# Optimization experiments

Measured on AMD Instinct MI355X. Metric: run time of the kernel, lower is better.

The kernel has to match this reference:

```python
import jax, jax.numpy as jnp
import numpy as np

BN_EPS = 1e-5

def _batchnorm(x, gamma, beta):
    # torch BatchNorm1d in training mode: batch mean, biased variance
    mean = jnp.mean(x, axis=0)
    var = jnp.mean(jnp.square(x - mean), axis=0)
    return (x - mean) * jax.lax.rsqrt(var + BN_EPS) * gamma + beta

def setup_inputs() -> dict:
    key = jax.random.key(0)
    ks = jax.random.split(key, 6)
    N, E, D_atom, D_nbr = 50000, 1600000, 64, 64
    d_in, d_out = 2 * D_atom + D_nbr, 2 * D_atom  # 192, 128
    return {
        "atom_in_fea": jax.random.normal(ks[0], (N, D_atom), dtype=jnp.float32),
        "nbr_fea": jax.random.normal(ks[1], (E, D_nbr), dtype=jnp.float32),
        "edge_src": jax.random.randint(ks[2], (E,), 0, N),
        "edge_dst": jax.random.randint(ks[3], (E,), 0, N),
        "W": jax.random.normal(ks[4], (d_in, d_out), dtype=jnp.float32) * (1.0 / np.sqrt(d_in)),
        "b": jax.random.normal(ks[5], (d_out,), dtype=jnp.float32) * 0.01,
        "bn1_gamma": jnp.ones((d_out,), dtype=jnp.float32),
        "bn1_beta": jnp.zeros((d_out,), dtype=jnp.float32),
        "bn2_gamma": jnp.ones((D_atom,), dtype=jnp.float32),
        "bn2_beta": jnp.zeros((D_atom,), dtype=jnp.float32),
    }

def reference(atom_in_fea, nbr_fea, edge_src, edge_dst, W, b,
              bn1_gamma, bn1_beta, bn2_gamma, bn2_beta):
    N, D = atom_in_fea.shape
    # gather endpoints, concat with edge features: [E, 2D + D_nbr]
    total_fea = jnp.concatenate(
        [atom_in_fea[edge_src], atom_in_fea[edge_dst], nbr_fea], axis=1)
    total_fea = _batchnorm(total_fea @ W + b, bn1_gamma, bn1_beta)
    filter_fea, core_fea = jnp.split(total_fea, 2, axis=1)
    nbr_msg = jax.nn.sigmoid(filter_fea) * jax.nn.softplus(core_fea)  # [E, D]
    # scatter-add messages to destination atoms
    atom_update = jax.ops.segment_sum(nbr_msg, edge_dst, num_segments=N)
    atom_update = _batchnorm(atom_update, bn2_gamma, bn2_beta)
    return jax.nn.softplus(atom_in_fea + atom_update)
```

## Files before the change

### kernel.cpp

```cpp
#include <hip/hip_runtime.h>
#include <hip/hip_bf16.h>

typedef __attribute__((ext_vector_type(8))) short short8;
typedef __attribute__((ext_vector_type(4))) float floatx4;
typedef __attribute__((ext_vector_type(4))) int intx4;
typedef __attribute__((ext_vector_type(4))) unsigned int uintx4;
typedef __attribute__((ext_vector_type(2))) float f32x2;

__device__ __forceinline__ float bits2f(unsigned short u) {
    union { unsigned int i; float f; } v; v.i = ((unsigned int)u) << 16; return v.f;
}
__device__ __forceinline__ unsigned short f2bb(float x) {
    union { float f; unsigned int i; } v; v.f = x;
    unsigned int r = v.i + 0x7FFFu + ((v.i >> 16) & 1u);
    return (unsigned short)(r >> 16);
}
__device__ __forceinline__ f32x2 unpk(unsigned int w) {
    union { unsigned int i; float f; } lo, hi;
    lo.i = w << 16;
    hi.i = w & 0xFFFF0000u;
    f32x2 r; r[0] = lo.f; r[1] = hi.f; return r;
}
__device__ __forceinline__ unsigned int pk2bb(float a, float b) {
    union { __hip_bfloat162 h; unsigned int u; } cv;
    cv.h = __float22bfloat162_rn(float2{a, b});
    return cv.u;
}
__device__ __forceinline__ float ldf(const void* base, long i, int fp32) {
    return fp32 ? ((const float*)base)[i] : bits2f(((const unsigned short*)base)[i]);
}
__device__ __forceinline__ short8 loadRow8(const void* base, long off, int fp32) {
    if (!fp32) {
        return *(const short8*)((const unsigned short*)base + off);
    }
    const float* f = (const float*)base + off;
    floatx4 f0 = *(const floatx4*)f;
    floatx4 f1 = *(const floatx4*)(f + 4);
    union { short8 s; uintx4 w; } o;
    o.w[0] = pk2bb(f0[0], f0[1]);
    o.w[1] = pk2bb(f0[2], f0[3]);
    o.w[2] = pk2bb(f1[0], f1[1]);
    o.w[3] = pk2bb(f1[2], f1[3]);
    return o.s;
}
__device__ __forceinline__ float lclamp(float z) {
    return fminf(fmaxf(z, -1e4f), 1e4f);
}

__global__ void k_probe(const unsigned short* __restrict__ Wb, int* __restrict__ flag) {
    int t = threadIdx.x;
    unsigned short u = Wb[t * 2];
    unsigned e = (u >> 7) & 0xFF;
    int in = (e >= 0x60 && e <= 0x8F) ? 1 : 0;
    unsigned long long m = __ballot(in);
    if (t == 0) flag[0] = (__popcll(m) < 32) ? 1 : 0;
}

__global__ __launch_bounds__(256) void k_atom_proj(
    const void* __restrict__ atom,
    const void* __restrict__ Wv,
    const void* __restrict__ bv,
    __hip_bfloat16* __restrict__ P, int N, const int* __restrict__ flagp)
{
    const int fp32 = *flagp;
    const int t = threadIdx.x;
    const int wave = t >> 6, lane = t & 63;
    const int half = wave & 1;
    const int pairInBlk = wave >> 1;
    const int n0 = lane & 15, kq = lane >> 4;
    unsigned short* Pu = (unsigned short*)P;

    short8 bf[8][2];
    #pragma unroll
    for (int tt = 0; tt < 8; ++tt)
        #pragma unroll
        for (int h = 0; h < 2; ++h)
            #pragma unroll
            for (int jj = 0; jj < 8; ++jj) {
                int k = half*64 + h*32 + kq*8 + jj;
                bf[tt][h][jj] = (short)f2bb(ldf(Wv, (long)k*128 + tt*16 + n0, fp32));
            }
    float bias[8];
    #pragma unroll
    for (int tt = 0; tt < 8; ++tt)
        bias[tt] = half ? 0.f : ldf(bv, tt*16 + n0, fp32);

    const long nGroups = ((long)N + 15) / 16;
    for (long g = (long)blockIdx.x*2 + pairInBlk; g < nGroups; g += (long)gridDim.x*2) {
        long a0 = g * 16;
        long am = a0 + n0;
        short8 a_lo = {}, a_hi = {};
        if (am < N) {
            a_lo = loadRow8(atom, am*64 + kq*8, fp32);
            a_hi = loadRow8(atom, am*64 + 32 + kq*8, fp32);
        }
        floatx4 acc[8];
        #pragma unroll
        for (int tt = 0; tt < 8; ++tt) {
            floatx4 c = {0.f, 0.f, 0.f, 0.f};
            c = __builtin_amdgcn_mfma_f32_16x16x32_bf16(a_lo, bf[tt][0], c, 0, 0, 0);
            c = __builtin_amdgcn_mfma_f32_16x16x32_bf16(a_hi, bf[tt][1], c, 0, 0, 0);
            acc[tt] = c;
        }
        #pragma unroll
        for (int r = 0; r < 4; ++r) {
            long a = a0 + kq*4 + r;
            if (a < N) {
                short8 v;
                #pragma unroll
                for (int tt = 0; tt < 8; ++tt)
                    v[tt] = (short)f2bb(lclamp(acc[tt][r] + bias[tt]));
                *(short8*)(Pu + a*256 + half*128 + n0*8) = v;
            }
        }
    }
}

template<int PHASE>
__global__ __launch_bounds__(256, 4) void k_edge(
    const void* __restrict__ nbr,
    const int* __restrict__ esrc,
    const int* __restrict__ edst,
    const void* __restrict__ Wv,
    const unsigned short* __restrict__ Pb,
    const float* __restrict__ coef,
    float* __restrict__ outAcc,
    long E, const int* __restrict__ flagp)
{
    __shared__ unsigned short s_w[8192];
    __shared__ float s_sum[128], s_ss[128];
    const int fp32 = *flagp;
    const int t = threadIdx.x;
    const int wave = t >> 6, lane = t & 63;
    const int n0 = lane & 15, kq = lane >> 4;

    for (int idx = t; idx < 8192; idx += 256) {
        int f  = idx >> 9;
        int l  = (idx >> 3) & 63;
        int jj = idx & 7;
        int tt = f >> 1, h = f & 1;
        int k = 128 + h*32 + (l >> 4)*8 + jj;
        s_w[idx] = f2bb(ldf(Wv, (long)k*128 + tt*16 + (l & 15), fp32));
    }
    if (PHASE == 0 && t < 128) { s_sum[t] = 0.f; s_ss[t] = 0.f; }
    __syncthreads();

    float sc[8], sh[8];
    if (PHASE == 1) {
        #pragma unroll
        for (int tt = 0; tt < 8; ++tt) {
            sc[tt] = coef[tt*16 + n0];
            sh[tt] = coef[128 + tt*16 + n0];
        }
    }
    f32x2 lsum2[4], lss2[4];
    if (PHASE == 0) {
        #pragma unroll
        for (int j = 0; j < 4; ++j) { lsum2[j] = f32x2{0.f, 0.f}; lss2[j] = f32x2{0.f, 0.f}; }
    }

    const unsigned short* swl = &s_w[lane * 8];

    const long nGroups = (E + 15) / 16;
    for (long g = (long)blockIdx.x*4 + wave; g < nGroups; g += (long)gridDim.x*4) {
        const long e0 = g * 16;
        const bool full = (e0 + 16 <= E);

        intx4 sv, dv;
        if (full) {
            sv = *(const intx4*)(esrc + e0 + kq*4);
            dv = *(const intx4*)(edst + e0 + kq*4);
        } else {
            #pragma unroll
            for (int r = 0; r < 4; ++r) {
                long er = e0 + kq*4 + r;
                sv[r] = (er < E) ? esrc[er] : 0;
                dv[r] = (er < E) ? edst[er] : 0;
            }
        }
        uintx4 vs[4], vd[4];
        #pragma unroll
        for (int r = 0; r < 4; ++r) {
            vs[r] = *(const uintx4*)(Pb + (long)sv[r]*256 + n0*8);
            vd[r] = *(const uintx4*)(Pb + (long)dv[r]*256 + 128 + n0*8);
        }
        long ea = e0 + n0;
        short8 a_lo = {}, a_hi = {};
        if (ea < E) {
            a_lo = loadRow8(nbr, ea*64 + kq*8, fp32);
            a_hi = loadRow8(nbr, ea*64 + 32 + kq*8, fp32);
        }
        floatx4 acc[8];
        #pragma unroll
        for (int tt = 0; tt < 8; ++tt) {
            short8 b0 = *(const short8*)(swl + (tt*2 + 0)*512);
            short8 b1 = *(const short8*)(swl + (tt*2 + 1)*512);
            floatx4 c = {0.f, 0.f, 0.f, 0.f};
            c = __builtin_amdgcn_mfma_f32_16x16x32_bf16(a_lo, b0, c, 0, 0, 0);
            c = __builtin_amdgcn_mfma_f32_16x16x32_bf16(a_hi, b1, c, 0, 0, 0);
            acc[tt] = c;
        }

        if (PHASE == 0) {
            if (full) {
                #pragma unroll
                for (int r = 0; r < 4; ++r)
                    #pragma unroll
                    for (int j = 0; j < 4; ++j) {
                        f32x2 ps = unpk(vs[r][j]);
                        f32x2 pd = unpk(vd[r][j]);
                        f32x2 a; a[0] = acc[2*j][r]; a[1] = acc[2*j+1][r];
                        f32x2 z = a + ps + pd;
                        lsum2[j] += z;
                        lss2[j]  += z * z;
                    }
            } else {
                #pragma unroll
                for (int r = 0; r < 4; ++r) {
                    long er = e0 + kq*4 + r;
                    if (er < E)
                        #pragma unroll
                        for (int j = 0; j < 4; ++j) {
                            f32x2 ps = unpk(vs[r][j]);
                            f32x2 pd = unpk(vd[r][j]);
                            f32x2 a; a[0] = acc[2*j][r]; a[1] = acc[2*j+1][r];
                            f32x2 z = a + ps + pd;
                            lsum2[j] += z;
                            lss2[j]  += z * z;
                        }
                }
            }
        } else {
            #pragma unroll
            for (int r = 0; r < 4; ++r) {
                long er = e0 + kq*4 + r;
                if (!full && er >= E) continue;
                f32x2 zh[4];
                #pragma unroll
                for (int j = 0; j < 4; ++j) {
                    f32x2 ps = unpk(vs[r][j]);
                    f32x2 pd = unpk(vd[r][j]);
                    f32x2 a;  a[0] = acc[2*j][r];  a[1] = acc[2*j+1][r];
                    f32x2 s2; s2[0] = sc[2*j];     s2[1] = sc[2*j+1];
                    f32x2 h2; h2[0] = sh[2*j];     h2[1] = sh[2*j+1];
                    zh[j] = (a + ps + pd) * s2 + h2;
                }
                float* ob = outAcc + (long)dv[r]*64 + n0;
                #pragma unroll
                for (int q = 0; q < 4; ++q) {
                    float f = zh[q >> 1][q & 1];
                    float c = zh[2 + (q >> 1)][q & 1];
                    float sig = __builtin_amdgcn_rcpf(1.f + __expf(-f));
                    float sp  = fmaxf(c, 0.f) + __logf(1.f + __expf(-fabsf(c)));
                    atomicAdd(ob + q*16, sig * sp);
                }
            }
        }
    }
    if (PHASE == 0) {
        __syncthreads();
        #pragma unroll
        for (int j = 0; j < 4; ++j) {
            atomicAdd(&s_sum[(2*j)*16 + n0],   lsum2[j][0]);
            atomicAdd(&s_sum[(2*j+1)*16 + n0], lsum2[j][1]);
            atomicAdd(&s_ss[(2*j)*16 + n0],    lss2[j][0]);
            atomicAdd(&s_ss[(2*j+1)*16 + n0],  lss2[j][1]);
        }
        __syncthreads();
        if (t < 128) {
            atomicAdd(&outAcc[t], s_sum[t]);
            atomicAdd(&outAcc[128 + t], s_ss[t]);
        }
    }
}

__global__ void k_fin1(const float* __restrict__ stats,
                       const void* __restrict__ gamma,
                       const void* __restrict__ beta,
                       float* __restrict__ coef, float invE,
                       const int* __restrict__ flagp)
{
    const int fp32 = *flagp;
    int t = threadIdx.x;
    float mean = stats[t] * invE;
    float var  = fmaxf(stats[128 + t] * invE - mean * mean, 0.f);
    float sc = ldf(gamma, t, fp32) * rsqrtf(var + 1e-5f);
    coef[t] = sc;
    coef[128 + t] = ldf(beta, t, fp32) - mean * sc;
}

__global__ void k_au_stats(const float* __restrict__ au, float* __restrict__ stats, int N)
{
    __shared__ float s_red[256];
    int t = threadIdx.x;
    int j = t & 63, r = t >> 6;
    float lsum = 0.f, lss = 0.f;
    for (int base = blockIdx.x * 4; base < N; base += gridDim.x * 4) {
        int a = base + r;
        if (a < N) { float v = au[(long)a*64 + j]; lsum += v; lss += v*v; }
    }
    s_red[t] = lsum; __syncthreads();
    if (t < 64) atomicAdd(&stats[j], s_red[j] + s_red[j+64] + s_red[j+128] + s_red[j+192]);
    __syncthreads();
    s_red[t] = lss; __syncthreads();
    if (t < 64) atomicAdd(&stats[64+j], s_red[j] + s_red[j+64] + s_red[j+128] + s_red[j+192]);
}

__global__ void k_fin2(const float* __restrict__ stats,
                       const void* __restrict__ gamma,
                       const void* __restrict__ beta,
                       float* __restrict__ coef, float invN,
                       const int* __restrict__ flagp)
{
    const int fp32 = *flagp;
    int t = threadIdx.x;
    float mean = stats[t] * invN;
    float var  = fmaxf(stats[64 + t] * invN - mean * mean, 0.f);
    float sc = ldf(gamma, t, fp32) * rsqrtf(var + 1e-5f);
    coef[t] = sc;
    coef[64 + t] = ldf(beta, t, fp32) - mean * sc;
}

__global__ void k_out(const void* __restrict__ atom,
                      const float* __restrict__ au,
                      const float* __restrict__ coef2,
                      void* __restrict__ out, long total,
                      const int* __restrict__ flagp)
{
    const int fp32 = *flagp;
    long i = (long)blockIdx.x * blockDim.x + threadIdx.x;
    if (i >= total) return;
    int j = (int)(i & 63);
    float x = lclamp(ldf(atom, i, fp32) + au[i] * coef2[j] + coef2[64 + j]);
    float sp = fmaxf(x, 0.f) + log1pf(__expf(-fabsf(x)));
    if (fp32) ((float*)out)[i] = sp;
    else      ((__hip_bfloat16*)out)[i] = __float2bfloat16(sp);
}

extern "C" void kernel_launch(void* const* d_in, const int* in_sizes, int n_in,
                              void* d_out, int out_size, void* d_ws, size_t ws_size,
                              hipStream_t stream)
{
    const void* atom = d_in[0];
    const void* nbr  = d_in[1];
    const int* esrc = (const int*)d_in[2];
    const int* edst = (const int*)d_in[3];
    const void* Wv  = d_in[4];
    const void* bv  = d_in[5];
    const void* g1  = d_in[6];
    const void* be1 = d_in[7];
    const void* g2  = d_in[8];
    const void* be2 = d_in[9];

    const int  N = in_sizes[0] / 64;
    const long E = (long)in_sizes[1] / 64;

    char* w = (char*)d_ws;
    __hip_bfloat16* P = (__hip_bfloat16*)w;  w += (size_t)N * 256 * sizeof(__hip_bfloat16);
    float* au     = (float*)w;               w += (size_t)N * 64 * sizeof(float);
    float* stats1 = (float*)w;               w += 256 * sizeof(float);
    float* stats2 = (float*)w;               w += 128 * sizeof(float);
    float* coef1  = (float*)w;               w += 256 * sizeof(float);
    float* coef2  = (float*)w;               w += 128 * sizeof(float);
    int* flagp    = (int*)w;

    hipMemsetAsync(au, 0, (size_t)N * 64 * sizeof(float), stream);
    hipMemsetAsync(stats1, 0, 384 * sizeof(float), stream);

    k_probe<<<1, 64, 0, stream>>>((const unsigned short*)Wv, flagp);
    k_atom_proj<<<1024, 256, 0, stream>>>(atom, Wv, bv, P, N, flagp);
    k_edge<0><<<2048, 256, 0, stream>>>(nbr, esrc, edst, Wv,
                                        (const unsigned short*)P, nullptr, stats1, E, flagp);
    k_fin1<<<1, 128, 0, stream>>>(stats1, g1, be1, coef1, 1.0f / (float)E, flagp);
    k_edge<1><<<2048, 256, 0, stream>>>(nbr, esrc, edst, Wv,
                                        (const unsigned short*)P, coef1, au, E, flagp);
    k_au_stats<<<1024, 256, 0, stream>>>(au, stats2, N);
    k_fin2<<<1, 64, 0, stream>>>(stats2, g2, be2, coef2, 1.0f / (float)N, flagp);
    long total = (long)N * 64;
    k_out<<<(int)((total + 255) / 256), 256, 0, stream>>>(atom, au, coef2,
                                                          d_out, total, flagp);
}
```

Measured before the change: 1.373 ms.

## Materialize pre-BN edge activations in bf16 and scatter from them in phase 2

The first edge pass now writes the pre-BatchNorm linear output z for every edge to workspace as bf16. When the workspace is large enough, the second pass becomes a lightweight scatter kernel that reads z and edst instead of re-gathering atom projections and nbr rows and redoing the MFMAs. The first pass is also unrolled to load two groups before computing them, to overlap gathers, and its occupancy bound drops to 3 blocks. The cost is an extra E×128 bf16 write and read of about 400MB of traffic, plus one more bf16 rounding of z before the activation.

Result: no change. 1.392 ms (+1.3%).

```diff
diff --git a/kernel.cpp b/kernel.cpp
--- a/kernel.cpp
+++ b/kernel.cpp
@@ -116,8 +116,172 @@
     }
 }
 
-template<int PHASE>
-__global__ __launch_bounds__(256, 4) void k_edge(
+#define LOADG(G, SV, DV, VS, VD, ALO, AHI, FULLV)                           \
+  {                                                                         \
+    const long e0_ = (G) * 16;                                              \
+    FULLV = (e0_ + 16 <= E);                                                \
+    if (FULLV) {                                                            \
+        SV = *(const intx4*)(esrc + e0_ + kq*4);                            \
+        DV = *(const intx4*)(edst + e0_ + kq*4);                            \
+    } else {                                                                \
+        _Pragma("unroll")                                                   \
+        for (int r = 0; r < 4; ++r) {                                       \
+            long er_ = e0_ + kq*4 + r;                                      \
+            SV[r] = (er_ < E) ? esrc[er_] : 0;                              \
+            DV[r] = (er_ < E) ? edst[er_] : 0;                              \
+        }                                                                   \
+    }                                                                       \
+    _Pragma("unroll")                                                       \
+    for (int r = 0; r < 4; ++r) {                                           \
+        VS[r] = *(const uintx4*)(Pb + (long)SV[r]*256 + n0*8);              \
+        VD[r] = *(const uintx4*)(Pb + (long)DV[r]*256 + 128 + n0*8);        \
+    }                                                                       \
+    long ea_ = e0_ + n0;                                                    \
+    ALO = short8{}; AHI = short8{};                                         \
+    if (ea_ < E) {                                                          \
+        ALO = loadRow8(nbr, ea_*64 + kq*8, fp32);                           \
+        AHI = loadRow8(nbr, ea_*64 + 32 + kq*8, fp32);                      \
+    }                                                                       \
+  }
+
+#define COMPG(G, VS, VD, ALO, AHI, FULLV)                                   \
+  {                                                                         \
+    const long e0_ = (G) * 16;                                              \
+    floatx4 acc_[8];                                                        \
+    _Pragma("unroll")                                                       \
+    for (int tt = 0; tt < 8; ++tt) {                                        \
+        short8 b0 = *(const short8*)(swl + (tt*2 + 0)*512);                 \
+        short8 b1 = *(const short8*)(swl + (tt*2 + 1)*512);                 \
+        floatx4 c = {0.f, 0.f, 0.f, 0.f};                                   \
+        c = __builtin_amdgcn_mfma_f32_16x16x32_bf16(ALO, b0, c, 0, 0, 0);   \
+        c = __builtin_amdgcn_mfma_f32_16x16x32_bf16(AHI, b1, c, 0, 0, 0);   \
+        acc_[tt] = c;                                                       \
+    }                                                                       \
+    _Pragma("unroll")                                                       \
+    for (int r = 0; r < 4; ++r) {                                           \
+        long er_ = e0_ + kq*4 + r;                                          \
+        if (FULLV || er_ < E) {                                             \
+            uintx4 zo;                                                      \
+            _Pragma("unroll")                                               \
+            for (int j = 0; j < 4; ++j) {                                   \
+                f32x2 ps = unpk(VS[r][j]);                                  \
+                f32x2 pd = unpk(VD[r][j]);                                  \
+                f32x2 a; a[0] = acc_[2*j][r]; a[1] = acc_[2*j+1][r];        \
+                f32x2 z = a + ps + pd;                                      \
+                lsum2[j] += z;                                              \
+                lss2[j]  += z * z;                                          \
+                zo[j] = pk2bb(z[0], z[1]);                                  \
+            }                                                               \
+            if (zw) *(uintx4*)(zw + er_*64 + n0*4) = zo;                    \
+        }                                                                   \
+    }                                                                       \
+  }
+
+__global__ __launch_bounds__(256, 3) void k_edge0(
+    const void* __restrict__ nbr,
+    const int* __restrict__ esrc,
+    const int* __restrict__ edst,
+    const void* __restrict__ Wv,
+    const unsigned short* __restrict__ Pb,
+    float* __restrict__ outAcc,
+    unsigned int* __restrict__ zw,
+    long E, const int* __restrict__ flagp)
+{
+    __shared__ unsigned short s_w[8192];
+    __shared__ float s_sum[128], s_ss[128];
+    const int fp32 = *flagp;
+    const int t = threadIdx.x;
+    const int wave = t >> 6, lane = t & 63;
+    const int n0 = lane & 15, kq = lane >> 4;
+
+    for (int idx = t; idx < 8192; idx += 256) {
+        int f  = idx >> 9;
+        int l  = (idx >> 3) & 63;
+        int jj = idx & 7;
+        int tt = f >> 1, h = f & 1;
+        int k = 128 + h*32 + (l >> 4)*8 + jj;
+        s_w[idx] = f2bb(ldf(Wv, (long)k*128 + tt*16 + (l & 15), fp32));
+    }
+    if (t < 128) { s_sum[t] = 0.f; s_ss[t] = 0.f; }
+    __syncthreads();
+
+    f32x2 lsum2[4], lss2[4];
+    #pragma unroll
+    for (int j = 0; j < 4; ++j) { lsum2[j] = f32x2{0.f, 0.f}; lss2[j] = f32x2{0.f, 0.f}; }
+
+    const unsigned short* swl = &s_w[lane * 8];
+
+    const long nGroups = (E + 15) / 16;
+    const long stride  = (long)gridDim.x * 4;
+    for (long g = (long)blockIdx.x*4 + wave; g < nGroups; g += 2*stride) {
+        long g2 = g + stride;
+        bool h2 = (g2 < nGroups);
+        bool fA = false, fB = false;
+        intx4 svA, dvA, svB, dvB;
+        uintx4 vsA[4], vdA[4], vsB[4], vdB[4];
+        short8 aloA, ahiA, aloB, ahiB;
+        LOADG(g, svA, dvA, vsA, vdA, aloA, ahiA, fA);
+        if (h2) LOADG(g2, svB, dvB, vsB, vdB, aloB, ahiB, fB);
+        COMPG(g, vsA, vdA, aloA, ahiA, fA);
+        if (h2) COMPG(g2, vsB, vdB, aloB, ahiB, fB);
+    }
+
+    __syncthreads();
+    #pragma unroll
+    for (int j = 0; j < 4; ++j) {
+        atomicAdd(&s_sum[(2*j)*16 + n0],   lsum2[j][0]);
+        atomicAdd(&s_sum[(2*j+1)*16 + n0], lsum2[j][1]);
+        atomicAdd(&s_ss[(2*j)*16 + n0],    lss2[j][0]);
+        atomicAdd(&s_ss[(2*j+1)*16 + n0],  lss2[j][1]);
+    }
+    __syncthreads();
+    if (t < 128) {
+        atomicAdd(&outAcc[t], s_sum[t]);
+        atomicAdd(&outAcc[128 + t], s_ss[t]);
+    }
+}
+
+__global__ __launch_bounds__(256) void k_scatter(
+    const unsigned int* __restrict__ zw,
+    const int* __restrict__ edst,
+    const float* __restrict__ coef,
+    float* __restrict__ au, long E)
+{
+    const int t = threadIdx.x;
+    const int n016 = t & 15;
+    float sc[8], sh[8];
+    #pragma unroll
+    for (int tt = 0; tt < 8; ++tt) {
+        sc[tt] = coef[tt*16 + n016];
+        sh[tt] = coef[128 + tt*16 + n016];
+    }
+    const long nUnits = E * 16;
+    const long gstep = (long)gridDim.x * blockDim.x;
+    for (long i = (long)blockIdx.x*blockDim.x + t; i < nUnits; i += gstep) {
+        long e = i >> 4;
+        uintx4 zv = *(const uintx4*)(zw + e*64 + n016*4);
+        int dst = edst[e];
+        f32x2 zh[4];
+        #pragma unroll
+        for (int j = 0; j < 4; ++j) {
+            f32x2 zz = unpk(zv[j]);
+            f32x2 s2; s2[0] = sc[2*j]; s2[1] = sc[2*j+1];
+            f32x2 h2; h2[0] = sh[2*j]; h2[1] = sh[2*j+1];
+            zh[j] = zz * s2 + h2;
+        }
+        float* ob = au + (long)dst*64 + n016;
+        #pragma unroll
+        for (int q = 0; q < 4; ++q) {
+            float f = zh[q >> 1][q & 1];
+            float c = zh[2 + (q >> 1)][q & 1];
+            float sig = __builtin_amdgcn_rcpf(1.f + __expf(-f));
+            float sp  = fmaxf(c, 0.f) + __logf(1.f + __expf(-fabsf(c)));
+            atomicAdd(ob + q*16, sig * sp);
+        }
+    }
+}
+
+__global__ __launch_bounds__(256, 4) void k_edge1(
     const void* __restrict__ nbr,
     const int* __restrict__ esrc,
     const int* __restrict__ edst,
@@ -128,7 +292,6 @@
     long E, const int* __restrict__ flagp)
 {
     __shared__ unsigned short s_w[8192];
-    __shared__ float s_sum[128], s_ss[128];
     const int fp32 = *flagp;
     const int t = threadIdx.x;
     const int wave = t >> 6, lane = t & 63;
@@ -142,21 +305,13 @@
         int k = 128 + h*32 + (l >> 4)*8 + jj;
         s_w[idx] = f2bb(ldf(Wv, (long)k*128 + tt*16 + (l & 15), fp32));
     }
-    if (PHASE == 0 && t < 128) { s_sum[t] = 0.f; s_ss[t] = 0.f; }
     __syncthreads();
 
     float sc[8], sh[8];
-    if (PHASE == 1) {
-        #pragma unroll
-        for (int tt = 0; tt < 8; ++tt) {
-            sc[tt] = coef[tt*16 + n0];
-            sh[tt] = coef[128 + tt*16 + n0];
-        }
-    }
-    f32x2 lsum2[4], lss2[4];
-    if (PHASE == 0) {
-        #pragma unroll
-        for (int j = 0; j < 4; ++j) { lsum2[j] = f32x2{0.f, 0.f}; lss2[j] = f32x2{0.f, 0.f}; }
+    #pragma unroll
+    for (int tt = 0; tt < 8; ++tt) {
+        sc[tt] = coef[tt*16 + n0];
+        sh[tt] = coef[128 + tt*16 + n0];
     }
 
     const unsigned short* swl = &s_w[lane * 8];
@@ -200,76 +355,29 @@
             c = __builtin_amdgcn_mfma_f32_16x16x32_bf16(a_hi, b1, c, 0, 0, 0);
             acc[tt] = c;
         }
-
-        if (PHASE == 0) {
-            if (full) {
-                #pragma unroll
-                for (int r = 0; r < 4; ++r)
-                    #pragma unroll
-                    for (int j = 0; j < 4; ++j) {
-                        f32x2 ps = unpk(vs[r][j]);
-                        f32x2 pd = unpk(vd[r][j]);
-                        f32x2 a; a[0] = acc[2*j][r]; a[1] = acc[2*j+1][r];
-                        f32x2 z = a + ps + pd;
-                        lsum2[j] += z;
-                        lss2[j]  += z * z;
-                    }
-            } else {
-                #pragma unroll
-                for (int r = 0; r < 4; ++r) {
-                    long er = e0 + kq*4 + r;
-                    if (er < E)
-                        #pragma unroll
-                        for (int j = 0; j < 4; ++j) {
-                            f32x2 ps = unpk(vs[r][j]);
-                            f32x2 pd = unpk(vd[r][j]);
-                            f32x2 a; a[0] = acc[2*j][r]; a[1] = acc[2*j+1][r];
-                            f32x2 z = a + ps + pd;
-                            lsum2[j] += z;
-                            lss2[j]  += z * z;
-                        }
-                }
+        #pragma unroll
+        for (int r = 0; r < 4; ++r) {
+            long er = e0 + kq*4 + r;
+            if (!full && er >= E) continue;
+            f32x2 zh[4];
+            #pragma unroll
+            for (int j = 0; j < 4; ++j) {
+                f32x2 ps = unpk(vs[r][j]);
+                f32x2 pd = unpk(vd[r][j]);
+                f32x2 a;  a[0] = acc[2*j][r];  a[1] = acc[2*j+1][r];
+                f32x2 s2; s2[0] = sc[2*j];     s2[1] = sc[2*j+1];
+                f32x2 h2; h2[0] = sh[2*j];     h2[1] = sh[2*j+1];
+                zh[j] = (a + ps + pd) * s2 + h2;
             }
-        } else {
+            float* ob = outAcc + (long)dv[r]*64 + n0;
             #pragma unroll
-            for (int r = 0; r < 4; ++r) {
-                long er = e0 + kq*4 + r;
-                if (!full && er >= E) continue;
-                f32x2 zh[4];
-                #pragma unroll
-                for (int j = 0; j < 4; ++j) {
-                    f32x2 ps = unpk(vs[r][j]);
-                    f32x2 pd = unpk(vd[r][j]);
-                    f32x2 a;  a[0] = acc[2*j][r];  a[1] = acc[2*j+1][r];
-                    f32x2 s2; s2[0] = sc[2*j];     s2[1] = sc[2*j+1];
-                    f32x2 h2; h2[0] = sh[2*j];     h2[1] = sh[2*j+1];
-                    zh[j] = (a + ps + pd) * s2 + h2;
-                }
-                float* ob = outAcc + (long)dv[r]*64 + n0;
-                #pragma unroll
-                for (int q = 0; q < 4; ++q) {
-                    float f = zh[q >> 1][q & 1];
-                    float c = zh[2 + (q >> 1)][q & 1];
-                    float sig = __builtin_amdgcn_rcpf(1.f + __expf(-f));
-                    float sp  = fmaxf(c, 0.f) + __logf(1.f + __expf(-fabsf(c)));
-                    atomicAdd(ob + q*16, sig * sp);
-                }
+            for (int q = 0; q < 4; ++q) {
+                float f = zh[q >> 1][q & 1];
+                float c = zh[2 + (q >> 1)][q & 1];
+                float sig = __builtin_amdgcn_rcpf(1.f + __expf(-f));
+                float sp  = fmaxf(c, 0.f) + __logf(1.f + __expf(-fabsf(c)));
+                atomicAdd(ob + q*16, sig * sp);
             }
-        }
-    }
-    if (PHASE == 0) {
-        __syncthreads();
-        #pragma unroll
-        for (int j = 0; j < 4; ++j) {
-            atomicAdd(&s_sum[(2*j)*16 + n0],   lsum2[j][0]);
-            atomicAdd(&s_sum[(2*j+1)*16 + n0], lsum2[j][1]);
-            atomicAdd(&s_ss[(2*j)*16 + n0],    lss2[j][0]);
-            atomicAdd(&s_ss[(2*j+1)*16 + n0],  lss2[j][1]);
-        }
-        __syncthreads();
-        if (t < 128) {
-            atomicAdd(&outAcc[t], s_sum[t]);
-            atomicAdd(&outAcc[128 + t], s_ss[t]);
         }
     }
 }
@@ -362,18 +470,28 @@
     float* stats2 = (float*)w;               w += 128 * sizeof(float);
     float* coef1  = (float*)w;               w += 256 * sizeof(float);
     float* coef2  = (float*)w;               w += 128 * sizeof(float);
-    int* flagp    = (int*)w;
+    int* flagp    = (int*)w;                 w += 256;
+
+    size_t zoff = (size_t)(w - (char*)d_ws);
+    zoff = (zoff + 255) & ~(size_t)255;
+    size_t zbytes = (size_t)E * 128 * sizeof(unsigned short);
+    bool useZ = (ws_size >= zoff + zbytes);
+    unsigned int* zw = useZ ? (unsigned int*)((char*)d_ws + zoff) : nullptr;
 
     hipMemsetAsync(au, 0, (size_t)N * 64 * sizeof(float), stream);
     hipMemsetAsync(stats1, 0, 384 * sizeof(float), stream);
 
     k_probe<<<1, 64, 0, stream>>>((const unsigned short*)Wv, flagp);
     k_atom_proj<<<1024, 256, 0, stream>>>(atom, Wv, bv, P, N, flagp);
-    k_edge<0><<<2048, 256, 0, stream>>>(nbr, esrc, edst, Wv,
-                                        (const unsigned short*)P, nullptr, stats1, E, flagp);
+    k_edge0<<<2048, 256, 0, stream>>>(nbr, esrc, edst, Wv,
+                                      (const unsigned short*)P, stats1, zw, E, flagp);
     k_fin1<<<1, 128, 0, stream>>>(stats1, g1, be1, coef1, 1.0f / (float)E, flagp);
-    k_edge<1><<<2048, 256, 0, stream>>>(nbr, esrc, edst, Wv,
-                                        (const unsigned short*)P, coef1, au, E, flagp);
+    if (useZ) {
+        k_scatter<<<2048, 256, 0, stream>>>(zw, edst, coef1, au, E);
+    } else {
+        k_edge1<<<2048, 256, 0, stream>>>(nbr, esrc, edst, Wv,
+                                          (const unsigned short*)P, coef1, au, E, flagp);
+    }
     k_au_stats<<<1024, 256, 0, stream>>>(au, stats2, N);
     k_fin2<<<1, 64, 0, stream>>>(stats2, g2, be2, coef2, 1.0f / (float)N, flagp);
     long total = (long)N * 64;
```
